# Kernel tuning notes

Measured on AMD Instinct MI355X. Metric: run time of the kernel, lower is better.

The kernel has to match this reference:

```python
import jax, jax.numpy as jnp
import numpy as np

IN_DIM, HID_DIM, CNV1_DIM, BATCH = 4096, 2048, 1024, 16384


def setup_inputs() -> dict:
    key = jax.random.key(0)
    ks = jax.random.split(key, 12)
    x = jax.random.normal(ks[0], (BATCH, IN_DIM), dtype=jnp.float32)
    mask_ih = jax.random.randint(ks[1], (HID_DIM, IN_DIM), 0, 2).astype(jnp.bool_)
    mask_hc = jax.random.randint(ks[2], (CNV1_DIM, HID_DIM), 0, 2).astype(jnp.bool_)
    # SparseLinear params (Linear-style: weight [out,in], bias [out])
    lim_ih = 1.0 / np.sqrt(IN_DIM)
    w_ih = jax.random.uniform(ks[3], (HID_DIM, IN_DIM), jnp.float32, -lim_ih, lim_ih)
    b_ih = jax.random.uniform(ks[4], (HID_DIM,), jnp.float32, -lim_ih, lim_ih)
    lim_hc = 1.0 / np.sqrt(HID_DIM)
    w_hc = jax.random.uniform(ks[5], (CNV1_DIM, HID_DIM), jnp.float32, -lim_hc, lim_hc)
    b_hc = jax.random.uniform(ks[6], (CNV1_DIM,), jnp.float32, -lim_hc, lim_hc)
    # Conv1d(1,1,2) weights, kaiming_uniform(tanh): gain=5/3, fan_in=2
    bound = (5.0 / 3.0) * np.sqrt(3.0 / 2.0)
    w_c1 = jax.random.uniform(ks[7], (2,), jnp.float32, -bound, bound)
    w_c2 = jax.random.uniform(ks[8], (2,), jnp.float32, -bound, bound)
    lim_c = 1.0 / np.sqrt(2.0)
    b_c1 = jax.random.uniform(ks[9], (), jnp.float32, -lim_c, lim_c)
    b_c2 = jax.random.uniform(ks[10], (), jnp.float32, -lim_c, lim_c)
    return {"x": x, "mask_ih": mask_ih, "mask_hc": mask_hc,
            "w_ih": w_ih, "b_ih": b_ih, "w_hc": w_hc, "b_hc": b_hc,
            "w_c1": w_c1, "b_c1": b_c1, "w_c2": w_c2, "b_c2": b_c2}


def _conv1d_k2s2(x, w, b):
    # Conv1d(1,1,kernel=2,stride=2) on [B, L] == pairwise reshape + dot
    B, L = x.shape
    return jnp.einsum('blk,k->bl', x.reshape(B, L // 2, 2), w) + b


def reference(x, mask_ih, mask_hc, w_ih, b_ih, w_hc, b_hc, w_c1, b_c1, w_c2, b_c2):
    h = jnp.tanh(x @ (w_ih * mask_ih).T + b_ih)            # [B, HID]
    c = jnp.tanh(h @ (w_hc * mask_hc).T + b_hc)            # [B, CNV1]
    y = jnp.tanh(_conv1d_k2s2(c, w_c1, b_c1))              # [B, CNV1/2]
    y = jnp.tanh(_conv1d_k2s2(y, w_c2, b_c2))              # [B, CNV1/4]
    return y
```

## Files before the change

### kernel.cpp

```cpp
#include <hip/hip_runtime.h>
#include <cstdint>
#include <cstddef>

typedef __bf16  bf16x8f __attribute__((ext_vector_type(8)));
typedef unsigned short u16x8 __attribute__((ext_vector_type(8)));
typedef float   f32x16 __attribute__((ext_vector_type(16)));

__device__ __forceinline__ unsigned short f2bf(float f) {
    union { float f; uint32_t u; } c; c.f = f;
    uint32_t u = c.u;
    return (unsigned short)((u + 0x7fffu + ((u >> 16) & 1u)) >> 16);
}

__device__ __forceinline__ float fast_tanh(float x) {
    float e = __builtin_exp2f(2.885390081777927f * x);
    return 1.0f - 2.0f * __builtin_amdgcn_rcpf(e + 1.0f);
}

__device__ __forceinline__ void load16_lds(const void* g, unsigned short* l) {
    __builtin_amdgcn_global_load_lds(
        (const __attribute__((address_space(1))) unsigned int*)g,
        (__attribute__((address_space(3))) unsigned int*)l,
        16, 0, 0);
}

__global__ __launch_bounds__(256)
void detect_mask(const unsigned char* __restrict__ m, int* __restrict__ flag) {
    __shared__ int s_gt1, s_off;
    if (threadIdx.x == 0) { s_gt1 = 0; s_off = 0; }
    __syncthreads();
    int gt1 = 0, off = 0;
    for (int k = threadIdx.x; k < 4096; k += 256) {
        unsigned char b = m[k];
        if (b > 1) gt1 = 1;
        if ((k & 3) && b) off = 1;
    }
    if (gt1) atomicOr(&s_gt1, 1);
    if (off) atomicOr(&s_off, 1);
    __syncthreads();
    if (threadIdx.x == 0) *flag = (!s_gt1 && s_off) ? 1 : 0;
}

__global__ __launch_bounds__(256)
void cast_f32_bf16(const float* __restrict__ in, unsigned short* __restrict__ out, int n) {
    int tid = blockIdx.x * blockDim.x + threadIdx.x;
    int stride = gridDim.x * blockDim.x;
    for (int e = tid * 4; e < n; e += stride * 4) {
        float4 v = *(const float4*)(in + e);
        ushort4 o;
        o.x = f2bf(v.x); o.y = f2bf(v.y); o.z = f2bf(v.z); o.w = f2bf(v.w);
        *(ushort4*)(out + e) = o;
    }
}

__global__ __launch_bounds__(256)
void mask_cast(const float* __restrict__ w, const void* __restrict__ mv,
               const int* __restrict__ flag, unsigned short* __restrict__ out, int n) {
    const bool u8 = (*flag != 0);
    int tid = blockIdx.x * blockDim.x + threadIdx.x;
    int stride = gridDim.x * blockDim.x;
    for (int e = tid * 4; e < n; e += stride * 4) {
        float4 v = *(const float4*)(w + e);
        int m0, m1, m2, m3;
        if (u8) {
            uchar4 mm = *(const uchar4*)((const unsigned char*)mv + e);
            m0 = mm.x; m1 = mm.y; m2 = mm.z; m3 = mm.w;
        } else {
            int4 mm = ((const int4*)mv)[e >> 2];
            m0 = mm.x; m1 = mm.y; m2 = mm.z; m3 = mm.w;
        }
        ushort4 o;
        o.x = m0 ? f2bf(v.x) : (unsigned short)0;
        o.y = m1 ? f2bf(v.y) : (unsigned short)0;
        o.z = m2 ? f2bf(v.z) : (unsigned short)0;
        o.w = m3 ? f2bf(v.w) : (unsigned short)0;
        *(ushort4*)(out + e) = o;
    }
}

template <typename OutT, bool FUSE>
__global__ __launch_bounds__(512, 2)
void gemm256(const unsigned short* __restrict__ A,
             const unsigned short* __restrict__ W,
             const float* __restrict__ bias,
             OutT* __restrict__ out,
             const float* __restrict__ w1, const float* __restrict__ b1,
             const float* __restrict__ w2, const float* __restrict__ b2,
             int N, int K, int lbx) {
    __shared__ __align__(16) unsigned short lds[65536];

    const int t    = threadIdx.x;
    const int lane = t & 63;
    const int wave = t >> 6;
    const int l31  = lane & 31;
    const int lh   = lane >> 5;
    const int wrow = (wave >> 2) * 128;
    const int wcol = (wave & 3) * 64;

    const int id = blockIdx.x;
    const int bx = (id >> 3) & ((1 << lbx) - 1);
    const int by = (id & 7) | ((id >> (3 + lbx)) << 3);
    const int bm = by * 256, bn = bx * 256;

    const char* Au = (const char*)(A + (size_t)bm * K);
    const char* Wu = (const char*)(W + (size_t)bn * K);

    uint32_t aSrc[2], bSrc[2][2];
#pragma unroll
    for (int j = 0; j < 2; ++j) {
        const int u = t + j * 512;
        { const int r = u >> 2, c = u & 3;
          aSrc[j] = (uint32_t)((r * K + ((c ^ ((r >> 1) & 3)) << 3)) * 2); }
        { const int rl = u >> 3, c = u & 7;
#pragma unroll
          for (int Un = 0; Un < 2; ++Un) {
              const int n = (rl & 31) + ((rl >> 5) << 6) + Un * 32;
              bSrc[Un][j] = (uint32_t)((n * K + ((c ^ (n & 7)) << 3)) * 2);
          } }
    }

    int aRow[4];
#pragma unroll
    for (int mt = 0; mt < 4; ++mt) aRow[mt] = (wrow + mt * 32 + l31) * 32;
    int aSwz[2];
#pragma unroll
    for (int j = 0; j < 2; ++j) aSwz[j] = ((j * 2 + lh) ^ ((l31 >> 1) & 3)) << 3;
    int bBase[2];
#pragma unroll
    for (int nt = 0; nt < 2; ++nt)
        bBase[nt] = 16384 + ((((wcol >> 5) + nt) & 1) * 8192)
                  + (((wcol + nt * 32) >> 6) * 2048) + l31 * 64;
    int bSwz[4];
#pragma unroll
    for (int kp = 0; kp < 2; ++kp)
#pragma unroll
        for (int j = 0; j < 2; ++j)
            bSwz[kp * 2 + j] = ((kp * 4 + j * 2 + lh) ^ (l31 & 7)) << 3;

#define STAGE_A(buf, Uk, kB) do {                                              \
    const char* g_ = Au + (kB);                                                \
    unsigned short* l_ = lds + (buf) * 32768 + (Uk) * 8192 + t * 8;            \
    load16_lds(g_ + aSrc[0] + (Uk) * 64, l_);                                  \
    load16_lds(g_ + aSrc[1] + (Uk) * 64, l_ + 4096);                           \
} while (0)

#define STAGE_B(buf, Un, kB) do {                                              \
    const char* g_ = Wu + (kB);                                                \
    unsigned short* l_ = lds + (buf) * 32768 + 16384 + (Un) * 8192 + t * 8;    \
    load16_lds(g_ + bSrc[Un][0], l_);                                          \
    load16_lds(g_ + bSrc[Un][1], l_ + 4096);                                   \
} while (0)

#define BAR    asm volatile("s_barrier" ::: "memory")
#define VMW2   asm volatile("s_waitcnt vmcnt(2)" ::: "memory")

#define PHASE(buf, kp, STAGE_STMT) do {                                        \
    u16x8 aF[4][2], bF[2][2];                                                  \
    const unsigned short* Lb_ = lds + (buf) * 32768;                           \
    _Pragma("unroll")                                                          \
    for (int j_ = 0; j_ < 2; ++j_) {                                           \
        _Pragma("unroll")                                                      \
        for (int mt_ = 0; mt_ < 4; ++mt_)                                      \
            aF[mt_][j_] = *(const u16x8*)(Lb_ + (kp) * 8192 + aRow[mt_] + aSwz[j_]); \
        _Pragma("unroll")                                                      \
        for (int nt_ = 0; nt_ < 2; ++nt_)                                      \
            bF[nt_][j_] = *(const u16x8*)(Lb_ + bBase[nt_] + bSwz[(kp) * 2 + j_]); \
    }                                                                          \
    STAGE_STMT;                                                                \
    __builtin_amdgcn_s_setprio(1);                                             \
    _Pragma("unroll")                                                          \
    for (int j_ = 0; j_ < 2; ++j_)                                             \
        _Pragma("unroll")                                                      \
        for (int mt_ = 0; mt_ < 4; ++mt_)                                      \
            _Pragma("unroll")                                                  \
            for (int nt_ = 0; nt_ < 2; ++nt_)                                  \
                acc[mt_][nt_] = __builtin_amdgcn_mfma_f32_32x32x16_bf16(       \
                    __builtin_bit_cast(bf16x8f, aF[mt_][j_]),                  \
                    __builtin_bit_cast(bf16x8f, bF[nt_][j_]),                  \
                    acc[mt_][nt_], 0, 0, 0);                                   \
    __builtin_amdgcn_s_setprio(0);                                             \
} while (0)

    f32x16 acc[4][2] = {};

    STAGE_A(0, 0, 0); STAGE_A(0, 1, 0); STAGE_B(0, 0, 0); STAGE_B(0, 1, 0);
    STAGE_A(1, 0, 128);
    VMW2;
    BAR;

    const int KB = K * 2;
    const int KL = KB - 128;
    for (int k0 = 0; k0 < KB; k0 += 256) {
        const int kO = k0 + 128;
        int kE2 = k0 + 256; if (kE2 > KL) kE2 = KL;
        int kO2 = k0 + 384; if (kO2 > KL) kO2 = KL;
        PHASE(0, 0, STAGE_A(1, 1, kO);  STAGE_B(1, 0, kO));        BAR;
        PHASE(0, 1, STAGE_B(1, 1, kO);  STAGE_A(0, 0, kE2)); VMW2; BAR;
        PHASE(1, 0, STAGE_A(0, 1, kE2); STAGE_B(0, 0, kE2));       BAR;
        PHASE(1, 1, STAGE_B(0, 1, kE2); STAGE_A(1, 0, kO2)); VMW2; BAR;
    }
    asm volatile("s_waitcnt vmcnt(0)" ::: "memory");

    float w10 = 0, w11 = 0, bb1 = 0, w20 = 0, w21 = 0, bb2 = 0;
    if constexpr (FUSE) {
        w10 = w1[0]; w11 = w1[1]; bb1 = b1[0];
        w20 = w2[0]; w21 = w2[1]; bb2 = b2[0];
    }
#pragma unroll
    for (int nt = 0; nt < 2; ++nt) {
        const int gn = bn + wcol + nt * 32 + l31;
        const float bv = bias[gn];
#pragma unroll
        for (int mt = 0; mt < 4; ++mt) {
#pragma unroll
            for (int reg = 0; reg < 16; ++reg) {
                const int gm = bm + wrow + mt * 32 + (reg & 3) + 8 * (reg >> 2) + 4 * lh;
                float c = fast_tanh(acc[mt][nt][reg] + bv);
                if constexpr (FUSE) {
                    float c1 = __shfl_xor(c, 1);
                    float c2 = __shfl_xor(c, 2);
                    float c3 = __shfl_xor(c, 3);
                    float y10 = fast_tanh(w10 * c  + w11 * c1 + bb1);
                    float y11 = fast_tanh(w10 * c2 + w11 * c3 + bb1);
                    float y   = fast_tanh(w20 * y10 + w21 * y11 + bb2);
                    if ((lane & 3) == 0)
                        out[(size_t)gm * (N >> 2) + (gn >> 2)] = (OutT)y;
                } else {
                    out[(size_t)gm * N + gn] = (OutT)f2bf(c);
                }
            }
        }
    }
#undef STAGE_A
#undef STAGE_B
#undef BAR
#undef VMW2
#undef PHASE
}

extern "C" void kernel_launch(void* const* d_in, const int* in_sizes, int n_in,
                              void* d_out, int out_size, void* d_ws, size_t ws_size,
                              hipStream_t stream) {
    constexpr int B   = 16384;
    constexpr int IN  = 4096;
    constexpr int HID = 2048;
    constexpr int CNV = 1024;

    const float* x       = (const float*)d_in[0];
    const void*  mask_ih = d_in[1];
    const void*  mask_hc = d_in[2];
    const float* w_ih    = (const float*)d_in[3];
    const float* b_ih    = (const float*)d_in[4];
    const float* w_hc    = (const float*)d_in[5];
    const float* b_hc    = (const float*)d_in[6];
    const float* w_c1    = (const float*)d_in[7];
    const float* b_c1    = (const float*)d_in[8];
    const float* w_c2    = (const float*)d_in[9];
    const float* b_c2    = (const float*)d_in[10];
    float* out = (float*)d_out;

    char* ws = (char*)d_ws;
    unsigned short* Xb  = (unsigned short*)(ws);
    unsigned short* Wih = (unsigned short*)(ws + 134217728);
    unsigned short* Whc = (unsigned short*)(ws + 150994944);
    unsigned short* Hb  = (unsigned short*)(ws + 155189248);
    int*            flag = (int*)(ws + 222298112);

    detect_mask<<<1, 256, 0, stream>>>((const unsigned char*)mask_ih, flag);

    cast_f32_bf16<<<4096, 256, 0, stream>>>(x, Xb, B * IN);
    mask_cast<<<1024, 256, 0, stream>>>(w_ih, mask_ih, flag, Wih, HID * IN);
    mask_cast<<<256, 256, 0, stream>>>(w_hc, mask_hc, flag, Whc, CNV * HID);

    gemm256<unsigned short, false><<<512, 512, 0, stream>>>(
        Xb, Wih, b_ih, Hb, nullptr, nullptr, nullptr, nullptr, HID, IN, 3);

    gemm256<float, true><<<256, 512, 0, stream>>>(
        Hb, Whc, b_hc, out, w_c1, b_c1, w_c2, b_c2, CNV, HID, 2);
}
```

Baseline: 799.8 us.

## Restructure GEMM main loop into triple-buffered K=32 stages with register double-buffering

Replaces the two-buffer, four-phase K=64 pipeline with a three-slot ring of K=32 LDS stages. The next fragments are read from LDS into a second register set while the MFMAs run on the current set. LDS shrinks from 128KB to 96KB and the A and W staging now share one uniform swizzle. The aim is to hide LDS read latency behind the MFMAs and to simplify the load scheduling, at the cost of more barriers per unit of K and more fragment registers.

```diff
diff --git a/kernel.cpp b/kernel.cpp
--- a/kernel.cpp
+++ b/kernel.cpp
@@ -87,7 +87,7 @@
              const float* __restrict__ w1, const float* __restrict__ b1,
              const float* __restrict__ w2, const float* __restrict__ b2,
              int N, int K, int lbx) {
-    __shared__ __align__(16) unsigned short lds[65536];
+    __shared__ __align__(16) unsigned short lds[49152];
 
     const int t    = threadIdx.x;
     const int lane = t & 63;
@@ -105,68 +105,51 @@
     const char* Au = (const char*)(A + (size_t)bm * K);
     const char* Wu = (const char*)(W + (size_t)bn * K);
 
-    uint32_t aSrc[2], bSrc[2][2];
+    uint32_t srcOff[2];
 #pragma unroll
     for (int j = 0; j < 2; ++j) {
-        const int u = t + j * 512;
-        { const int r = u >> 2, c = u & 3;
-          aSrc[j] = (uint32_t)((r * K + ((c ^ ((r >> 1) & 3)) << 3)) * 2); }
-        { const int rl = u >> 3, c = u & 7;
-#pragma unroll
-          for (int Un = 0; Un < 2; ++Un) {
-              const int n = (rl & 31) + ((rl >> 5) << 6) + Un * 32;
-              bSrc[Un][j] = (uint32_t)((n * K + ((c ^ (n & 7)) << 3)) * 2);
-          } }
-    }
-
-    int aRow[4];
-#pragma unroll
-    for (int mt = 0; mt < 4; ++mt) aRow[mt] = (wrow + mt * 32 + l31) * 32;
-    int aSwz[2];
-#pragma unroll
-    for (int j = 0; j < 2; ++j) aSwz[j] = ((j * 2 + lh) ^ ((l31 >> 1) & 3)) << 3;
-    int bBase[2];
-#pragma unroll
-    for (int nt = 0; nt < 2; ++nt)
-        bBase[nt] = 16384 + ((((wcol >> 5) + nt) & 1) * 8192)
-                  + (((wcol + nt * 32) >> 6) * 2048) + l31 * 64;
-    int bSwz[4];
-#pragma unroll
-    for (int kp = 0; kp < 2; ++kp)
+        const int u = t + j * 512, r = u >> 2, c = u & 3;
+        srcOff[j] = (uint32_t)((r * K + ((c ^ ((r >> 1) & 3)) << 3)) * 2);
+    }
+
+    int aAddr[4][2], bAddr[2][2];
+#pragma unroll
+    for (int mt = 0; mt < 4; ++mt) {
+        const int row = wrow + mt * 32 + l31;
 #pragma unroll
         for (int j = 0; j < 2; ++j)
-            bSwz[kp * 2 + j] = ((kp * 4 + j * 2 + lh) ^ (l31 & 7)) << 3;
-
-#define STAGE_A(buf, Uk, kB) do {                                              \
-    const char* g_ = Au + (kB);                                                \
-    unsigned short* l_ = lds + (buf) * 32768 + (Uk) * 8192 + t * 8;            \
-    load16_lds(g_ + aSrc[0] + (Uk) * 64, l_);                                  \
-    load16_lds(g_ + aSrc[1] + (Uk) * 64, l_ + 4096);                           \
+            aAddr[mt][j] = row * 32 + (((j * 2 + lh) ^ ((row >> 1) & 3)) << 3);
+    }
+#pragma unroll
+    for (int nt = 0; nt < 2; ++nt) {
+        const int row = wcol + nt * 32 + l31;
+#pragma unroll
+        for (int j = 0; j < 2; ++j)
+            bAddr[nt][j] = 8192 + row * 32 + (((j * 2 + lh) ^ ((row >> 1) & 3)) << 3);
+    }
+
+#define STAGE(slotS, kB) do {                                                  \
+    unsigned short* la_ = lds + (slotS) + t * 8;                               \
+    load16_lds(Au + (kB) + srcOff[0], la_);                                    \
+    load16_lds(Au + (kB) + srcOff[1], la_ + 4096);                             \
+    load16_lds(Wu + (kB) + srcOff[0], la_ + 8192);                             \
+    load16_lds(Wu + (kB) + srcOff[1], la_ + 12288);                            \
 } while (0)
 
-#define STAGE_B(buf, Un, kB) do {                                              \
-    const char* g_ = Wu + (kB);                                                \
-    unsigned short* l_ = lds + (buf) * 32768 + 16384 + (Un) * 8192 + t * 8;    \
-    load16_lds(g_ + bSrc[Un][0], l_);                                          \
-    load16_lds(g_ + bSrc[Un][1], l_ + 4096);                                   \
-} while (0)
-
-#define BAR    asm volatile("s_barrier" ::: "memory")
-#define VMW2   asm volatile("s_waitcnt vmcnt(2)" ::: "memory")
-
-#define PHASE(buf, kp, STAGE_STMT) do {                                        \
-    u16x8 aF[4][2], bF[2][2];                                                  \
-    const unsigned short* Lb_ = lds + (buf) * 32768;                           \
+#define RDAH(FA, FB, base) do {                                                \
+    const unsigned short* Lb_ = lds + (base);                                  \
     _Pragma("unroll")                                                          \
     for (int j_ = 0; j_ < 2; ++j_) {                                           \
         _Pragma("unroll")                                                      \
         for (int mt_ = 0; mt_ < 4; ++mt_)                                      \
-            aF[mt_][j_] = *(const u16x8*)(Lb_ + (kp) * 8192 + aRow[mt_] + aSwz[j_]); \
+            FA[mt_][j_] = *(const u16x8*)(Lb_ + aAddr[mt_][j_]);               \
         _Pragma("unroll")                                                      \
         for (int nt_ = 0; nt_ < 2; ++nt_)                                      \
-            bF[nt_][j_] = *(const u16x8*)(Lb_ + bBase[nt_] + bSwz[(kp) * 2 + j_]); \
+            FB[nt_][j_] = *(const u16x8*)(Lb_ + bAddr[nt_][j_]);               \
     }                                                                          \
-    STAGE_STMT;                                                                \
+} while (0)
+
+#define MM(FA, FB) do {                                                        \
     __builtin_amdgcn_s_setprio(1);                                             \
     _Pragma("unroll")                                                          \
     for (int j_ = 0; j_ < 2; ++j_)                                             \
@@ -175,29 +158,44 @@
             _Pragma("unroll")                                                  \
             for (int nt_ = 0; nt_ < 2; ++nt_)                                  \
                 acc[mt_][nt_] = __builtin_amdgcn_mfma_f32_32x32x16_bf16(       \
-                    __builtin_bit_cast(bf16x8f, aF[mt_][j_]),                  \
-                    __builtin_bit_cast(bf16x8f, bF[nt_][j_]),                  \
+                    __builtin_bit_cast(bf16x8f, FA[mt_][j_]),                  \
+                    __builtin_bit_cast(bf16x8f, FB[nt_][j_]),                  \
                     acc[mt_][nt_], 0, 0, 0);                                   \
     __builtin_amdgcn_s_setprio(0);                                             \
 } while (0)
 
+#define VMW4 asm volatile("s_waitcnt vmcnt(4)" ::: "memory")
+#define BAR  asm volatile("s_barrier" ::: "memory")
+
     f32x16 acc[4][2] = {};
-
-    STAGE_A(0, 0, 0); STAGE_A(0, 1, 0); STAGE_B(0, 0, 0); STAGE_B(0, 1, 0);
-    STAGE_A(1, 0, 128);
-    VMW2;
+    u16x8 fa0[4][2], fb0[2][2], fa1[4][2], fb1[2][2];
+
+    STAGE(0, 0);
+    STAGE(16384, 64);
+    VMW4;
     BAR;
-
-    const int KB = K * 2;
-    const int KL = KB - 128;
-    for (int k0 = 0; k0 < KB; k0 += 256) {
-        const int kO = k0 + 128;
-        int kE2 = k0 + 256; if (kE2 > KL) kE2 = KL;
-        int kO2 = k0 + 384; if (kO2 > KL) kO2 = KL;
-        PHASE(0, 0, STAGE_A(1, 1, kO);  STAGE_B(1, 0, kO));        BAR;
-        PHASE(0, 1, STAGE_B(1, 1, kO);  STAGE_A(0, 0, kE2)); VMW2; BAR;
-        PHASE(1, 0, STAGE_A(0, 1, kE2); STAGE_B(0, 0, kE2));       BAR;
-        PHASE(1, 1, STAGE_B(0, 1, kE2); STAGE_A(1, 0, kO2)); VMW2; BAR;
+    RDAH(fa0, fb0, 0);
+
+    uint32_t sOld = 0, sRd = 16384, sSt = 32768;
+    const int KBt = K * 2;
+    const int KL  = KBt - 64;
+    for (int kb = 0; kb < KBt; kb += 128) {
+        int k1 = kb + 128; if (k1 > KL) k1 = KL;
+        int k2 = kb + 192; if (k2 > KL) k2 = KL;
+        STAGE(sSt, k1);
+        VMW4;
+        BAR;
+        RDAH(fa1, fb1, sRd);
+        MM(fa0, fb0);
+        BAR;
+        { uint32_t tmp = sOld; sOld = sRd; sRd = sSt; sSt = tmp; }
+        STAGE(sSt, k2);
+        VMW4;
+        BAR;
+        RDAH(fa0, fb0, sRd);
+        MM(fa1, fb1);
+        BAR;
+        { uint32_t tmp = sOld; sOld = sRd; sRd = sSt; sSt = tmp; }
     }
     asm volatile("s_waitcnt vmcnt(0)" ::: "memory");
 
@@ -231,11 +229,11 @@
             }
         }
     }
-#undef STAGE_A
-#undef STAGE_B
+#undef STAGE
+#undef RDAH
+#undef MM
+#undef VMW4
 #undef BAR
-#undef VMW2
-#undef PHASE
 }
 
 extern "C" void kernel_launch(void* const* d_in, const int* in_sizes, int n_in,
```

Result: no change. 814.5 us (+1.8%).
